# Kernel optimization log

Hardware: AMD Instinct MI355X
Metric: run time of the kernel (lower is better)

## Reference

```python
import jax, jax.numpy as jnp
import numpy as np

NUM_HEADS = 12


def setup_inputs() -> dict:
    key = jax.random.key(0)
    k_x, k_m, k_qkv, k_proj = jax.random.split(key, 4)
    B, N, C = 2, 2048, 768
    x = jax.random.normal(k_x, (B, N, C), dtype=jnp.float32)
    # binary key mask: 1 = attend, 0 = masked out
    mask = jax.random.randint(k_m, (B, N), 0, 2).astype(jnp.int32)
    # torch Linear(dim, dim*3, bias=False): stored here as [in, out]
    w_qkv = jax.random.normal(k_qkv, (C, 3 * C), dtype=jnp.float32) * 0.02
    w_proj = jax.random.normal(k_proj, (C, C), dtype=jnp.float32) * 0.02
    b_proj = jnp.zeros((C,), dtype=jnp.float32)
    return {"x": x, "mask": mask, "w_qkv": w_qkv, "w_proj": w_proj, "b_proj": b_proj}


def reference(x, mask, w_qkv, w_proj, b_proj):
    B, N, C = x.shape
    H = NUM_HEADS
    hd = C // H
    scale = hd ** -0.5
    qkv = (x @ w_qkv).reshape(B, N, 3, H, hd)
    q, k, v = jnp.moveaxis(qkv, 2, 0)            # each [B, N, H, hd]
    attn = jnp.einsum('bnhd,bmhd->bhnm', q, k) * scale  # [B, H, N, N]
    # faithful masked_softmax: unstable exp (no max subtraction), mask keys, renormalize
    m = mask.astype(x.dtype)[:, None, None, :]   # [B, 1, 1, N]
    x_exp = jnp.exp(attn) * m
    attn = x_exp / x_exp.sum(-1, keepdims=True)
    out = jnp.einsum('bhnm,bmhd->bnhd', attn, v).reshape(B, N, C)
    return out @ w_proj + b_proj
```

## Files before the change

kernel.cpp:

```cpp
#include <hip/hip_runtime.h>
#include <cstdint>

#define NB 2
#define NSEQ 2048
#define CDIM 768
#define NH 12
#define HD 64
#define NTOK (NB*NSEQ)
#define QKV_COLS (3*CDIM)
#define NBLK ((NSEQ/64)*NH*NB)

typedef short bf16x8 __attribute__((ext_vector_type(8)));
typedef short bf16x4 __attribute__((ext_vector_type(4)));
typedef float f32x4  __attribute__((ext_vector_type(4)));
typedef short short4v __attribute__((ext_vector_type(4)));
typedef unsigned int uint4v __attribute__((ext_vector_type(4)));

#define MFMA16(a,b,c) __builtin_amdgcn_mfma_f32_16x16x32_bf16(a,b,c,0,0,0)

__device__ __forceinline__ short f2b(float f) {
    uint32_t u = __builtin_bit_cast(uint32_t, f);
    u += 0x7fffu + ((u >> 16) & 1u);
    return (short)(u >> 16);
}
__device__ __forceinline__ unsigned pack2(float a, float b) {
    unsigned ua = __builtin_bit_cast(unsigned, a) + 0x7fffu;
    unsigned ub = __builtin_bit_cast(unsigned, b) + 0x7fffu;
    return __builtin_amdgcn_perm(ub, ua, 0x07060302u);
}
__device__ __forceinline__ void gll16(const short* g, short* l) {
    __builtin_amdgcn_global_load_lds(
        (const __attribute__((address_space(1))) unsigned int*)g,
        (__attribute__((address_space(3))) unsigned int*)l, 16, 0, 0);
}

__global__ __launch_bounds__(256) void prep_kernel(
    const float* __restrict__ x, const float* __restrict__ w_qkv,
    const float* __restrict__ w_proj,
    short* __restrict__ xb, short* __restrict__ wqt, short* __restrict__ wpt)
{
    __shared__ float tile[32][33];
    const int bid = blockIdx.x, t = threadIdx.x;
    if (bid < 3072) {
        int i = bid * 256 + t;
        float4 v = ((const float4*)x)[i];
        short4v o = { f2b(v.x), f2b(v.y), f2b(v.z), f2b(v.w) };
        ((short4v*)xb)[i] = o;
        return;
    }
    const float* w; short* wt; int K, NC, n0, k0;
    if (bid < 3072 + 1728) {
        int r = bid - 3072;
        w = w_qkv; wt = wqt; K = CDIM; NC = QKV_COLS;
        n0 = (r % 72) * 32; k0 = (r / 72) * 32;
    } else {
        int r = bid - 4800;
        w = w_proj; wt = wpt; K = CDIM; NC = CDIM;
        n0 = (r % 24) * 32; k0 = (r / 24) * 32;
    }
    #pragma unroll
    for (int i = 0; i < 4; ++i) {
        int idx = t + i * 256; int r = idx >> 5, c = idx & 31;
        tile[r][c] = w[(size_t)(k0 + r) * NC + n0 + c];
    }
    __syncthreads();
    #pragma unroll
    for (int i = 0; i < 4; ++i) {
        int idx = t + i * 256; int r = idx >> 5, c = idx & 31;
        wt[(size_t)(n0 + r) * K + k0 + c] = f2b(tile[c][r]);
    }
}

__global__ __launch_bounds__(256) void gemm_qkv(
    const short* __restrict__ A ,
    const short* __restrict__ B ,
    short* __restrict__ qb, short* __restrict__ kb, short* __restrict__ vt)
{
    __shared__ short As[128 * 32];
    __shared__ short Bs[128 * 32];
    const int t = threadIdx.x;
    const int lane = t & 63, wid = t >> 6;
    const int quad = lane >> 4, l16 = lane & 15;
    const int wA = wid >> 1, wB = wid & 1;
    const int n0 = blockIdx.x * 128;
    const int m0 = blockIdx.y * 128;

    const int srow = wid * 16 + (lane >> 2), schunk = (lane & 3) * 8;
    const short* ag0 = A + (size_t)(n0 + srow) * CDIM + schunk;
    const short* ag1 = ag0 + (size_t)64 * CDIM;
    const short* bg0 = B + (size_t)(m0 + srow) * CDIM + schunk;
    const short* bg1 = bg0 + (size_t)64 * CDIM;
    short* asl0 = &As[(wid * 16) * 32];
    short* asl1 = &As[(wid * 16 + 64) * 32];
    short* bsl0 = &Bs[(wid * 16) * 32];
    short* bsl1 = &Bs[(wid * 16 + 64) * 32];

    f32x4 acc[4][4] = {};
    for (int k0 = 0; k0 < CDIM; k0 += 32) {
        __syncthreads();
        gll16(ag0 + k0, asl0);
        gll16(ag1 + k0, asl1);
        gll16(bg0 + k0, bsl0);
        gll16(bg1 + k0, bsl1);
        __syncthreads();
        bf16x8 af[4], bf[4];
        #pragma unroll
        for (int i = 0; i < 4; ++i)
            af[i] = *(const bf16x8*)&As[(wA*64 + i*16 + l16) * 32 + quad*8];
        #pragma unroll
        for (int j = 0; j < 4; ++j)
            bf[j] = *(const bf16x8*)&Bs[(wB*64 + j*16 + l16) * 32 + quad*8];
        #pragma unroll
        for (int i = 0; i < 4; ++i)
            #pragma unroll
            for (int j = 0; j < 4; ++j)
                acc[i][j] = MFMA16(af[i], bf[j], acc[i][j]);
    }

    const int colbase = n0 + wA * 64;
    const int s = colbase / CDIM;
    const int h = (colbase - s * CDIM) >> 6;
    const int b = m0 >> 11;
    const size_t bh = (size_t)(b * NH + h);
    const float qsc = (s == 0) ? 0.125f : 1.0f;
    #pragma unroll
    for (int i = 0; i < 4; ++i) {
        const int d0 = i*16 + quad*4;
        #pragma unroll
        for (int j = 0; j < 4; ++j) {
            int tok = (m0 + wB*64 + j*16 + l16) & (NSEQ - 1);
            if (s < 2) {
                short* dst = (s == 0 ? qb : kb) + (bh * NSEQ + tok) * HD + d0;
                short4v o = { f2b(acc[i][j][0] * qsc), f2b(acc[i][j][1] * qsc),
                              f2b(acc[i][j][2] * qsc), f2b(acc[i][j][3] * qsc) };
                *(short4v*)dst = o;
            } else {
                short* dst = vt + (bh * HD + d0) * NSEQ + tok;
                #pragma unroll
                for (int r = 0; r < 4; ++r)
                    dst[(size_t)r * NSEQ] = f2b(acc[i][j][r]);
            }
        }
    }
}

#define STAGE(KT, BUF) do {                                                      \
    short* kb_ = (BUF);                                                          \
    short* vb_ = (BUF) + 8192;                                                   \
    _Pragma("unroll")                                                            \
    for (int j = 0; j < 4; ++j) {                                                \
        gll16(kp + (size_t)((KT) + rK[j]) * HD + cK[j]*8,                        \
              kb_ + wid*2048 + j*512);                                           \
        gll16(vp + (size_t)dV[j] * NSEQ + (KT) + cV[j]*8,                        \
              vb_ + wid*2048 + j*512);                                           \
    }                                                                            \
} while (0)

#define BODY(KT, BUF) do {                                                       \
    const short* KsB_ = (BUF);                                                   \
    const short* VsB_ = (BUF) + 8192;                                            \
    int4 mi0_ = *(const int4*)(mp + (KT) + kbase);                               \
    int4 mi1_ = *(const int4*)(mp + (KT) + 64 + kbase);                          \
    bf16x8 kf00_ = *(const bf16x8*)&KsB_[krow + kc0];                            \
    bf16x8 kf01_ = *(const bf16x8*)&KsB_[krow + kc1];                            \
    bf16x8 kf10_ = *(const bf16x8*)&KsB_[4096 + krow + kc0];                     \
    bf16x8 kf11_ = *(const bf16x8*)&KsB_[4096 + krow + kc1];                     \
    f32x4 s0_[4] = {}, s1_[4] = {};                                              \
    _Pragma("unroll")                                                            \
    for (int jt = 0; jt < 4; ++jt) {                                             \
        s0_[jt] = MFMA16(kf00_, qf[jt][0], s0_[jt]);                             \
        s0_[jt] = MFMA16(kf01_, qf[jt][1], s0_[jt]);                             \
        s1_[jt] = MFMA16(kf10_, qf[jt][0], s1_[jt]);                             \
        s1_[jt] = MFMA16(kf11_, qf[jt][1], s1_[jt]);                             \
    }                                                                            \
    float4 m0_ = {(float)mi0_.x, (float)mi0_.y, (float)mi0_.z, (float)mi0_.w};   \
    float4 m1_ = {(float)mi1_.x, (float)mi1_.y, (float)mi1_.z, (float)mi1_.w};   \
    bf16x8 pb_[4];                                                               \
    _Pragma("unroll")                                                            \
    for (int jt = 0; jt < 4; ++jt) {                                             \
        float e0 = __expf(s0_[jt][0]) * m0_.x;                                   \
        float e1 = __expf(s0_[jt][1]) * m0_.y;                                   \
        float e2 = __expf(s0_[jt][2]) * m0_.z;                                   \
        float e3 = __expf(s0_[jt][3]) * m0_.w;                                   \
        float f0 = __expf(s1_[jt][0]) * m1_.x;                                   \
        float f1 = __expf(s1_[jt][1]) * m1_.y;                                   \
        float f2 = __expf(s1_[jt][2]) * m1_.z;                                   \
        float f3 = __expf(s1_[jt][3]) * m1_.w;                                   \
        l[jt] += ((e0 + e1) + (e2 + e3)) + ((f0 + f1) + (f2 + f3));              \
        uint4v pk_ = { pack2(e0, e1), pack2(e2, e3),                             \
                       pack2(f0, f1), pack2(f2, f3) };                           \
        pb_[jt] = __builtin_bit_cast(bf16x8, pk_);                               \
    }                                                                            \
    _Pragma("unroll")                                                            \
    for (int it = 0; it < 4; ++it) {                                             \
        const int vrow_ = (it*16 + l16) * 128;                                   \
        bf16x4 lo_ = *(const bf16x4*)&VsB_[vrow_ + vposl + vsub];                \
        bf16x4 hi_ = *(const bf16x4*)&VsB_[vrow_ + vposh + vsub];                \
        bf16x8 vf_ = __builtin_shufflevector(lo_, hi_, 0,1,2,3,4,5,6,7);         \
        _Pragma("unroll")                                                        \
        for (int jt = 0; jt < 4; ++jt)                                           \
            o_acc[it][jt] = MFMA16(vf_, pb_[jt], o_acc[it][jt]);                 \
    }                                                                            \
} while (0)

__global__ __launch_bounds__(256, 2) void attn_kernel(
    const short* __restrict__ qb, const short* __restrict__ kb,
    const short* __restrict__ vt, const int* __restrict__ mask,
    short* __restrict__ ao)
{
    __shared__ __align__(16) short KV[2][16384];
    float (*Ob)[68] = (float(*)[68])KV;
    float (*lsum)[64] = (float(*)[64])((char*)KV + 17408);

    const int t = threadIdx.x;
    const int lane = t & 63, wid = t >> 6;
    const int quad = lane >> 4, l16 = lane & 15;
    const int id = blockIdx.x;
    const int idx = id >> 3;
    const int bh = (id & 7) + ((idx % 3) << 3);
    const int q0 = (idx / 3) << 6;
    const int b = bh / NH, h = bh - b * NH;
    const size_t hoff = (size_t)bh * NSEQ * HD;
    const short* qp = qb + hoff;
    const short* kp = kb + hoff;
    const short* vp = vt + hoff;
    const int* mp = mask + b * NSEQ;
    const int kbase = wid * 16 + quad * 4;

    int rK[4], cK[4], dV[4], cV[4];
    #pragma unroll
    for (int j = 0; j < 4; ++j) {
        int o = wid * 4096 + j * 1024 + lane * 16;
        rK[j] = o >> 7;
        cK[j] = ((o >> 4) & 7) ^ (rK[j] & 7);
        dV[j] = o >> 8;
        cV[j] = ((o >> 4) & 15) ^ (dV[j] & 15);
    }
    const int r7 = l16 & 7;
    const int krow = (wid * 16 + l16) * 64;
    const int kc0 = ((quad     ^ r7) << 3);
    const int kc1 = (((quad+4) ^ r7) << 3);
    const int vposl = ((wid*2 + (quad >> 1)) ^ l16) << 3;
    const int vposh = (((8 + wid*2 + (quad >> 1)) ^ l16) << 3);
    const int vsub = (quad & 1) * 4;

    bf16x8 qf[4][2];
    #pragma unroll
    for (int jt = 0; jt < 4; ++jt) {
        const short* qr = qp + (size_t)(q0 + jt*16 + l16) * HD + quad*8;
        qf[jt][0] = *(const bf16x8*)qr;
        qf[jt][1] = *(const bf16x8*)(qr + 32);
    }

    f32x4 o_acc[4][4] = {};
    float l[4] = {0.f, 0.f, 0.f, 0.f};

    STAGE(0, KV[0]);
    __syncthreads();

    for (int kt = 0; kt < NSEQ; kt += 256) {
        STAGE(kt + 128, KV[1]);
        BODY(kt, KV[0]);
        __syncthreads();
        const int nx = (kt + 256) & (NSEQ - 1);
        STAGE(nx, KV[0]);
        BODY(kt + 128, KV[1]);
        __syncthreads();
    }

    #pragma unroll
    for (int jt = 0; jt < 4; ++jt) {
        l[jt] += __shfl_xor(l[jt], 16);
        l[jt] += __shfl_xor(l[jt], 32);
        if (quad == 0) lsum[wid][jt*16 + l16] = l[jt];
    }
    for (int w = 0; w < 4; ++w) {
        __syncthreads();
        if (wid == w) {
            #pragma unroll
            for (int it = 0; it < 4; ++it)
                #pragma unroll
                for (int jt = 0; jt < 4; ++jt)
                    #pragma unroll
                    for (int r = 0; r < 4; ++r) {
                        if (w == 0)
                            Ob[it*16 + quad*4 + r][jt*16 + l16] = o_acc[it][jt][r];
                        else
                            Ob[it*16 + quad*4 + r][jt*16 + l16] += o_acc[it][jt][r];
                    }
        }
    }
    __syncthreads();

    {
        const int ql = t >> 2, dc = (t & 3) * 16;
        float inv = 1.0f / (((lsum[0][ql] + lsum[1][ql]) +
                             (lsum[2][ql] + lsum[3][ql])));
        bf16x8 o8a, o8b;
        #pragma unroll
        for (int d = 0; d < 8; ++d) o8a[d] = f2b(Ob[dc + d][ql] * inv);
        #pragma unroll
        for (int d = 0; d < 8; ++d) o8b[d] = f2b(Ob[dc + 8 + d][ql] * inv);
        int tok = b * NSEQ + q0 + ql;
        short* dst = ao + (size_t)tok * CDIM + h * HD + dc;
        *(bf16x8*)dst = o8a;
        *(bf16x8*)(dst + 8) = o8b;
    }
}

__global__ __launch_bounds__(256) void gemm_proj(
    const short* __restrict__ A ,
    const short* __restrict__ B ,
    const float* __restrict__ bias, float* __restrict__ out)
{
    __shared__ short As[128 * 32];
    __shared__ short Bs[128 * 32];
    const int t = threadIdx.x;
    const int lane = t & 63, wid = t >> 6;
    const int quad = lane >> 4, l16 = lane & 15;
    const int wA = wid >> 1, wB = wid & 1;
    const int n0 = blockIdx.x * 128;
    const int m0 = blockIdx.y * 128;

    const int srow = wid * 16 + (lane >> 2), schunk = (lane & 3) * 8;
    const short* ag0 = A + (size_t)(n0 + srow) * CDIM + schunk;
    const short* ag1 = ag0 + (size_t)64 * CDIM;
    const short* bg0 = B + (size_t)(m0 + srow) * CDIM + schunk;
    const short* bg1 = bg0 + (size_t)64 * CDIM;
    short* asl0 = &As[(wid * 16) * 32];
    short* asl1 = &As[(wid * 16 + 64) * 32];
    short* bsl0 = &Bs[(wid * 16) * 32];
    short* bsl1 = &Bs[(wid * 16 + 64) * 32];

    f32x4 acc[4][4] = {};
    for (int k0 = 0; k0 < CDIM; k0 += 32) {
        __syncthreads();
        gll16(ag0 + k0, asl0);
        gll16(ag1 + k0, asl1);
        gll16(bg0 + k0, bsl0);
        gll16(bg1 + k0, bsl1);
        __syncthreads();
        bf16x8 af[4], bf[4];
        #pragma unroll
        for (int i = 0; i < 4; ++i)
            af[i] = *(const bf16x8*)&As[(wA*64 + i*16 + l16) * 32 + quad*8];
        #pragma unroll
        for (int j = 0; j < 4; ++j)
            bf[j] = *(const bf16x8*)&Bs[(wB*64 + j*16 + l16) * 32 + quad*8];
        #pragma unroll
        for (int i = 0; i < 4; ++i)
            #pragma unroll
            for (int j = 0; j < 4; ++j)
                acc[i][j] = MFMA16(af[i], bf[j], acc[i][j]);
    }

    #pragma unroll
    for (int i = 0; i < 4; ++i) {
        int col0 = n0 + wA*64 + i*16 + quad*4;
        float4 bias4 = *(const float4*)&bias[col0];
        #pragma unroll
        for (int j = 0; j < 4; ++j) {
            int tok = m0 + wB*64 + j*16 + l16;
            float4 o = { acc[i][j][0] + bias4.x, acc[i][j][1] + bias4.y,
                         acc[i][j][2] + bias4.z, acc[i][j][3] + bias4.w };
            *(float4*)(out + (size_t)tok * CDIM + col0) = o;
        }
    }
}

extern "C" void kernel_launch(void* const* d_in, const int* in_sizes, int n_in,
                              void* d_out, int out_size, void* d_ws, size_t ws_size,
                              hipStream_t stream)
{
    const float* x      = (const float*)d_in[0];
    const int*   mask   = (const int*)d_in[1];
    const float* w_qkv  = (const float*)d_in[2];
    const float* w_proj = (const float*)d_in[3];
    const float* b_proj = (const float*)d_in[4];
    float* out = (float*)d_out;

    const size_t SZ = (size_t)NTOK * CDIM;
    short* xb  = (short*)d_ws;
    short* wqt = xb  + SZ;
    short* wpt = wqt + (size_t)QKV_COLS * CDIM;
    short* qb  = wpt + (size_t)CDIM * CDIM;
    short* kb  = qb  + SZ;
    short* vt  = kb  + SZ;
    short* ao  = vt  + SZ;

    dim3 blk(256);
    prep_kernel<<<dim3(5376), blk, 0, stream>>>(x, w_qkv, w_proj, xb, wqt, wpt);
    gemm_qkv<<<dim3(QKV_COLS/128, NTOK/128), blk, 0, stream>>>(wqt, xb, qb, kb, vt);
    attn_kernel<<<dim3(NBLK), blk, 0, stream>>>(qb, kb, vt, mask, ao);
    gemm_proj<<<dim3(CDIM/128, NTOK/128), blk, 0, stream>>>(wpt, ao, b_proj, out);
}
```

Before: 177.1 us.

## Load attention K/V fragments directly from global into registers, drop LDS staging

The attention kernel no longer stages K and V tiles through double-buffered shared memory with async global-to-LDS loads and barriers. Each wave now loads its K fragments straight into registers, double-buffered in software, and reads its V fragments from global memory inside the body. The mask is converted to float once in the prep kernel so the inner loop skips int-to-float conversion. This removes the per-tile __syncthreads and the LDS traffic, at the cost of more global and L2 traffic and higher register pressure, since each wave re-reads K/V that were previously shared across the block.

```diff
diff --git a/kernel.cpp b/kernel.cpp
--- a/kernel.cpp
+++ b/kernel.cpp
@@ -36,8 +36,9 @@
 
 __global__ __launch_bounds__(256) void prep_kernel(
     const float* __restrict__ x, const float* __restrict__ w_qkv,
-    const float* __restrict__ w_proj,
-    short* __restrict__ xb, short* __restrict__ wqt, short* __restrict__ wpt)
+    const float* __restrict__ w_proj, const int* __restrict__ mask,
+    short* __restrict__ xb, short* __restrict__ wqt, short* __restrict__ wpt,
+    float* __restrict__ maskf)
 {
     __shared__ float tile[32][33];
     const int bid = blockIdx.x, t = threadIdx.x;
@@ -46,6 +47,13 @@
         float4 v = ((const float4*)x)[i];
         short4v o = { f2b(v.x), f2b(v.y), f2b(v.z), f2b(v.w) };
         ((short4v*)xb)[i] = o;
+        return;
+    }
+    if (bid >= 5376) {
+        int i = ((bid - 5376) << 10) + (t << 2);
+        int4 mi = *(const int4*)(mask + i);
+        float4 mo = { (float)mi.x, (float)mi.y, (float)mi.z, (float)mi.w };
+        *(float4*)(maskf + i) = mo;
         return;
     }
     const float* w; short* wt; int K, NC, n0, k0;
@@ -144,37 +152,32 @@
     }
 }
 
-#define STAGE(KT, BUF) do {                                                      \
-    short* kb_ = (BUF);                                                          \
-    short* vb_ = (BUF) + 8192;                                                   \
+#define LOADK(KT, KF) do {                                                       \
+    const short* kt_ = kbase + (size_t)(KT) * HD;                                \
+    KF[0] = *(const bf16x8*)(kt_);                                               \
+    KF[1] = *(const bf16x8*)(kt_ + 32);                                          \
+    KF[2] = *(const bf16x8*)(kt_ + 64*HD);                                       \
+    KF[3] = *(const bf16x8*)(kt_ + 64*HD + 32);                                  \
+} while (0)
+
+#define BODY(KT, KF) do {                                                        \
+    bf16x4 vlo_[4], vhi_[4];                                                     \
     _Pragma("unroll")                                                            \
-    for (int j = 0; j < 4; ++j) {                                                \
-        gll16(kp + (size_t)((KT) + rK[j]) * HD + cK[j]*8,                        \
-              kb_ + wid*2048 + j*512);                                           \
-        gll16(vp + (size_t)dV[j] * NSEQ + (KT) + cV[j]*8,                        \
-              vb_ + wid*2048 + j*512);                                           \
+    for (int it = 0; it < 4; ++it) {                                             \
+        const short* vr_ = vbase + (size_t)(it*16) * NSEQ + (KT);                \
+        vlo_[it] = *(const bf16x4*)(vr_);                                        \
+        vhi_[it] = *(const bf16x4*)(vr_ + 64);                                   \
     }                                                                            \
-} while (0)
-
-#define BODY(KT, BUF) do {                                                       \
-    const short* KsB_ = (BUF);                                                   \
-    const short* VsB_ = (BUF) + 8192;                                            \
-    int4 mi0_ = *(const int4*)(mp + (KT) + kbase);                               \
-    int4 mi1_ = *(const int4*)(mp + (KT) + 64 + kbase);                          \
-    bf16x8 kf00_ = *(const bf16x8*)&KsB_[krow + kc0];                            \
-    bf16x8 kf01_ = *(const bf16x8*)&KsB_[krow + kc1];                            \
-    bf16x8 kf10_ = *(const bf16x8*)&KsB_[4096 + krow + kc0];                     \
-    bf16x8 kf11_ = *(const bf16x8*)&KsB_[4096 + krow + kc1];                     \
+    float4 m0_ = *(const float4*)(mp + (KT) + mbase);                            \
+    float4 m1_ = *(const float4*)(mp + (KT) + 64 + mbase);                       \
     f32x4 s0_[4] = {}, s1_[4] = {};                                              \
     _Pragma("unroll")                                                            \
     for (int jt = 0; jt < 4; ++jt) {                                             \
-        s0_[jt] = MFMA16(kf00_, qf[jt][0], s0_[jt]);                             \
-        s0_[jt] = MFMA16(kf01_, qf[jt][1], s0_[jt]);                             \
-        s1_[jt] = MFMA16(kf10_, qf[jt][0], s1_[jt]);                             \
-        s1_[jt] = MFMA16(kf11_, qf[jt][1], s1_[jt]);                             \
+        s0_[jt] = MFMA16(KF[0], qf[jt][0], s0_[jt]);                             \
+        s0_[jt] = MFMA16(KF[1], qf[jt][1], s0_[jt]);                             \
+        s1_[jt] = MFMA16(KF[2], qf[jt][0], s1_[jt]);                             \
+        s1_[jt] = MFMA16(KF[3], qf[jt][1], s1_[jt]);                             \
     }                                                                            \
-    float4 m0_ = {(float)mi0_.x, (float)mi0_.y, (float)mi0_.z, (float)mi0_.w};   \
-    float4 m1_ = {(float)mi1_.x, (float)mi1_.y, (float)mi1_.z, (float)mi1_.w};   \
     bf16x8 pb_[4];                                                               \
     _Pragma("unroll")                                                            \
     for (int jt = 0; jt < 4; ++jt) {                                             \
@@ -193,10 +196,8 @@
     }                                                                            \
     _Pragma("unroll")                                                            \
     for (int it = 0; it < 4; ++it) {                                             \
-        const int vrow_ = (it*16 + l16) * 128;                                   \
-        bf16x4 lo_ = *(const bf16x4*)&VsB_[vrow_ + vposl + vsub];                \
-        bf16x4 hi_ = *(const bf16x4*)&VsB_[vrow_ + vposh + vsub];                \
-        bf16x8 vf_ = __builtin_shufflevector(lo_, hi_, 0,1,2,3,4,5,6,7);         \
+        bf16x8 vf_ = __builtin_shufflevector(vlo_[it], vhi_[it],                 \
+                                             0,1,2,3,4,5,6,7);                   \
         _Pragma("unroll")                                                        \
         for (int jt = 0; jt < 4; ++jt)                                           \
             o_acc[it][jt] = MFMA16(vf_, pb_[jt], o_acc[it][jt]);                 \
@@ -205,12 +206,11 @@
 
 __global__ __launch_bounds__(256, 2) void attn_kernel(
     const short* __restrict__ qb, const short* __restrict__ kb,
-    const short* __restrict__ vt, const int* __restrict__ mask,
+    const short* __restrict__ vt, const float* __restrict__ maskf,
     short* __restrict__ ao)
 {
-    __shared__ __align__(16) short KV[2][16384];
-    float (*Ob)[68] = (float(*)[68])KV;
-    float (*lsum)[64] = (float(*)[64])((char*)KV + 17408);
+    __shared__ __align__(16) float Ob[64][68];
+    __shared__ float lsum[4][64];
 
     const int t = threadIdx.x;
     const int lane = t & 63, wid = t >> 6;
@@ -224,25 +224,11 @@
     const short* qp = qb + hoff;
     const short* kp = kb + hoff;
     const short* vp = vt + hoff;
-    const int* mp = mask + b * NSEQ;
-    const int kbase = wid * 16 + quad * 4;
-
-    int rK[4], cK[4], dV[4], cV[4];
-    #pragma unroll
-    for (int j = 0; j < 4; ++j) {
-        int o = wid * 4096 + j * 1024 + lane * 16;
-        rK[j] = o >> 7;
-        cK[j] = ((o >> 4) & 7) ^ (rK[j] & 7);
-        dV[j] = o >> 8;
-        cV[j] = ((o >> 4) & 15) ^ (dV[j] & 15);
-    }
-    const int r7 = l16 & 7;
-    const int krow = (wid * 16 + l16) * 64;
-    const int kc0 = ((quad     ^ r7) << 3);
-    const int kc1 = (((quad+4) ^ r7) << 3);
-    const int vposl = ((wid*2 + (quad >> 1)) ^ l16) << 3;
-    const int vposh = (((8 + wid*2 + (quad >> 1)) ^ l16) << 3);
-    const int vsub = (quad & 1) * 4;
+    const float* mp = maskf + b * NSEQ;
+    const int mbase = wid * 16 + quad * 4;
+
+    const short* kbase = kp + (size_t)(wid*16 + l16) * HD + quad*8;
+    const short* vbase = vp + (size_t)l16 * NSEQ + wid*16 + quad*4;
 
     bf16x8 qf[4][2];
     #pragma unroll
@@ -255,17 +241,13 @@
     f32x4 o_acc[4][4] = {};
     float l[4] = {0.f, 0.f, 0.f, 0.f};
 
-    STAGE(0, KV[0]);
-    __syncthreads();
-
+    bf16x8 kA[4], kB[4];
+    LOADK(0, kA);
     for (int kt = 0; kt < NSEQ; kt += 256) {
-        STAGE(kt + 128, KV[1]);
-        BODY(kt, KV[0]);
-        __syncthreads();
-        const int nx = (kt + 256) & (NSEQ - 1);
-        STAGE(nx, KV[0]);
-        BODY(kt + 128, KV[1]);
-        __syncthreads();
+        LOADK(kt + 128, kB);
+        BODY(kt, kA);
+        LOADK((kt + 256) & (NSEQ - 1), kA);
+        BODY(kt + 128, kB);
     }
 
     #pragma unroll
@@ -387,10 +369,12 @@
     short* kb  = qb  + SZ;
     short* vt  = kb  + SZ;
     short* ao  = vt  + SZ;
+    float* maskf = (float*)(ao + SZ);
 
     dim3 blk(256);
-    prep_kernel<<<dim3(5376), blk, 0, stream>>>(x, w_qkv, w_proj, xb, wqt, wpt);
+    prep_kernel<<<dim3(5380), blk, 0, stream>>>(x, w_qkv, w_proj, mask,
+                                                xb, wqt, wpt, maskf);
     gemm_qkv<<<dim3(QKV_COLS/128, NTOK/128), blk, 0, stream>>>(wqt, xb, qb, kb, vt);
-    attn_kernel<<<dim3(NBLK), blk, 0, stream>>>(qb, kb, vt, mask, ao);
+    attn_kernel<<<dim3(NBLK), blk, 0, stream>>>(qb, kb, vt, maskf, ao);
     gemm_proj<<<dim3(CDIM/128, NTOK/128), blk, 0, stream>>>(wpt, ao, b_proj, out);
 }
```

Result: slower. 210.0 us (+18.6%).

## Split K/V staging, single-buffer V, cache bf16 mask in LDS for occupancy

Applied to the files above, without the earlier changes.

The attention kernel's shared memory is restructured. K stays double-buffered while V gets a single buffer that is loaded at the start of each tile and consumed after an added barrier. The key mask is converted to bf16 in the prep kernel and staged once per block into LDS, replacing per-tile global int loads. LDS per block drops, so launch bounds rise to 3 blocks per CU for more occupancy. The cost is twice as many barriers per tile and V loads that are now exposed rather than prefetched a tile ahead.

```diff
diff --git a/kernel.cpp b/kernel.cpp
--- a/kernel.cpp
+++ b/kernel.cpp
@@ -23,6 +23,9 @@
     u += 0x7fffu + ((u >> 16) & 1u);
     return (short)(u >> 16);
 }
+__device__ __forceinline__ float b2f(short s) {
+    return __builtin_bit_cast(float, (uint32_t)((uint32_t)(unsigned short)s << 16));
+}
 __device__ __forceinline__ unsigned pack2(float a, float b) {
     unsigned ua = __builtin_bit_cast(unsigned, a) + 0x7fffu;
     unsigned ub = __builtin_bit_cast(unsigned, b) + 0x7fffu;
@@ -36,8 +39,9 @@
 
 __global__ __launch_bounds__(256) void prep_kernel(
     const float* __restrict__ x, const float* __restrict__ w_qkv,
-    const float* __restrict__ w_proj,
-    short* __restrict__ xb, short* __restrict__ wqt, short* __restrict__ wpt)
+    const float* __restrict__ w_proj, const int* __restrict__ mask,
+    short* __restrict__ xb, short* __restrict__ wqt, short* __restrict__ wpt,
+    short* __restrict__ maskb)
 {
     __shared__ float tile[32][33];
     const int bid = blockIdx.x, t = threadIdx.x;
@@ -46,6 +50,18 @@
         float4 v = ((const float4*)x)[i];
         short4v o = { f2b(v.x), f2b(v.y), f2b(v.z), f2b(v.w) };
         ((short4v*)xb)[i] = o;
+        return;
+    }
+    if (bid >= 5376) {
+        int i = ((bid - 5376) << 11) + (t << 3);
+        int4 a = *(const int4*)(mask + i);
+        int4 c = *(const int4*)(mask + i + 4);
+        short4v o0 = { f2b((float)a.x), f2b((float)a.y),
+                       f2b((float)a.z), f2b((float)a.w) };
+        short4v o1 = { f2b((float)c.x), f2b((float)c.y),
+                       f2b((float)c.z), f2b((float)c.w) };
+        *(short4v*)(maskb + i) = o0;
+        *(short4v*)(maskb + i + 4) = o1;
         return;
     }
     const float* w; short* wt; int K, NC, n0, k0;
@@ -144,23 +160,25 @@
     }
 }
 
-#define STAGE(KT, BUF) do {                                                      \
+#define STAGE_K(KT, BUF) do {                                                    \
     short* kb_ = (BUF);                                                          \
-    short* vb_ = (BUF) + 8192;                                                   \
     _Pragma("unroll")                                                            \
-    for (int j = 0; j < 4; ++j) {                                                \
+    for (int j = 0; j < 4; ++j)                                                  \
         gll16(kp + (size_t)((KT) + rK[j]) * HD + cK[j]*8,                        \
               kb_ + wid*2048 + j*512);                                           \
+} while (0)
+
+#define STAGE_V(KT) do {                                                         \
+    _Pragma("unroll")                                                            \
+    for (int j = 0; j < 4; ++j)                                                  \
         gll16(vp + (size_t)dV[j] * NSEQ + (KT) + cV[j]*8,                        \
-              vb_ + wid*2048 + j*512);                                           \
-    }                                                                            \
+              Vb + wid*2048 + j*512);                                            \
 } while (0)
 
-#define BODY(KT, BUF) do {                                                       \
-    const short* KsB_ = (BUF);                                                   \
-    const short* VsB_ = (BUF) + 8192;                                            \
-    int4 mi0_ = *(const int4*)(mp + (KT) + kbase);                               \
-    int4 mi1_ = *(const int4*)(mp + (KT) + 64 + kbase);                          \
+#define QKBODY(KT, KBUF) do {                                                    \
+    const short* KsB_ = (KBUF);                                                  \
+    short4v mi0_ = *(const short4v*)&Msk[(KT) + mbase];                          \
+    short4v mi1_ = *(const short4v*)&Msk[(KT) + 64 + mbase];                     \
     bf16x8 kf00_ = *(const bf16x8*)&KsB_[krow + kc0];                            \
     bf16x8 kf01_ = *(const bf16x8*)&KsB_[krow + kc1];                            \
     bf16x8 kf10_ = *(const bf16x8*)&KsB_[4096 + krow + kc0];                     \
@@ -173,9 +191,8 @@
         s1_[jt] = MFMA16(kf10_, qf[jt][0], s1_[jt]);                             \
         s1_[jt] = MFMA16(kf11_, qf[jt][1], s1_[jt]);                             \
     }                                                                            \
-    float4 m0_ = {(float)mi0_.x, (float)mi0_.y, (float)mi0_.z, (float)mi0_.w};   \
-    float4 m1_ = {(float)mi1_.x, (float)mi1_.y, (float)mi1_.z, (float)mi1_.w};   \
-    bf16x8 pb_[4];                                                               \
+    float4 m0_ = { b2f(mi0_[0]), b2f(mi0_[1]), b2f(mi0_[2]), b2f(mi0_[3]) };     \
+    float4 m1_ = { b2f(mi1_[0]), b2f(mi1_[1]), b2f(mi1_[2]), b2f(mi1_[3]) };     \
     _Pragma("unroll")                                                            \
     for (int jt = 0; jt < 4; ++jt) {                                             \
         float e0 = __expf(s0_[jt][0]) * m0_.x;                                   \
@@ -189,28 +206,33 @@
         l[jt] += ((e0 + e1) + (e2 + e3)) + ((f0 + f1) + (f2 + f3));              \
         uint4v pk_ = { pack2(e0, e1), pack2(e2, e3),                             \
                        pack2(f0, f1), pack2(f2, f3) };                           \
-        pb_[jt] = __builtin_bit_cast(bf16x8, pk_);                               \
+        pb[jt] = __builtin_bit_cast(bf16x8, pk_);                                \
     }                                                                            \
+} while (0)
+
+#define PVBODY() do {                                                            \
     _Pragma("unroll")                                                            \
     for (int it = 0; it < 4; ++it) {                                             \
         const int vrow_ = (it*16 + l16) * 128;                                   \
-        bf16x4 lo_ = *(const bf16x4*)&VsB_[vrow_ + vposl + vsub];                \
-        bf16x4 hi_ = *(const bf16x4*)&VsB_[vrow_ + vposh + vsub];                \
+        bf16x4 lo_ = *(const bf16x4*)&Vb[vrow_ + vposl + vsub];                  \
+        bf16x4 hi_ = *(const bf16x4*)&Vb[vrow_ + vposh + vsub];                  \
         bf16x8 vf_ = __builtin_shufflevector(lo_, hi_, 0,1,2,3,4,5,6,7);         \
         _Pragma("unroll")                                                        \
         for (int jt = 0; jt < 4; ++jt)                                           \
-            o_acc[it][jt] = MFMA16(vf_, pb_[jt], o_acc[it][jt]);                 \
+            o_acc[it][jt] = MFMA16(vf_, pb[jt], o_acc[it][jt]);                  \
     }                                                                            \
 } while (0)
 
-__global__ __launch_bounds__(256, 2) void attn_kernel(
+__global__ __launch_bounds__(256, 3) void attn_kernel(
     const short* __restrict__ qb, const short* __restrict__ kb,
-    const short* __restrict__ vt, const int* __restrict__ mask,
+    const short* __restrict__ vt, const short* __restrict__ maskb,
     short* __restrict__ ao)
 {
-    __shared__ __align__(16) short KV[2][16384];
-    float (*Ob)[68] = (float(*)[68])KV;
-    float (*lsum)[64] = (float(*)[64])((char*)KV + 17408);
+    __shared__ __align__(16) short Kb[2][8192];
+    __shared__ __align__(16) short Vb[8192];
+    __shared__ __align__(16) short Msk[2048];
+    float (*Ob)[68] = (float(*)[68])Kb;
+    float (*lsum)[64] = (float(*)[64])((char*)Kb + 17408);
 
     const int t = threadIdx.x;
     const int lane = t & 63, wid = t >> 6;
@@ -224,8 +246,7 @@
     const short* qp = qb + hoff;
     const short* kp = kb + hoff;
     const short* vp = vt + hoff;
-    const int* mp = mask + b * NSEQ;
-    const int kbase = wid * 16 + quad * 4;
+    const int mbase = wid * 16 + quad * 4;
 
     int rK[4], cK[4], dV[4], cV[4];
     #pragma unroll
@@ -254,17 +275,25 @@
 
     f32x4 o_acc[4][4] = {};
     float l[4] = {0.f, 0.f, 0.f, 0.f};
-
-    STAGE(0, KV[0]);
+    bf16x8 pb[4];
+
+    STAGE_K(0, Kb[0]);
+    gll16(maskb + b * NSEQ + t * 8, Msk + wid * 512);
     __syncthreads();
 
     for (int kt = 0; kt < NSEQ; kt += 256) {
-        STAGE(kt + 128, KV[1]);
-        BODY(kt, KV[0]);
-        __syncthreads();
-        const int nx = (kt + 256) & (NSEQ - 1);
-        STAGE(nx, KV[0]);
-        BODY(kt + 128, KV[1]);
+        STAGE_V(kt);
+        STAGE_K(kt + 128, Kb[1]);
+        QKBODY(kt, Kb[0]);
+        __syncthreads();
+        PVBODY();
+        __syncthreads();
+
+        STAGE_V(kt + 128);
+        STAGE_K((kt + 256) & (NSEQ - 1), Kb[0]);
+        QKBODY(kt + 128, Kb[1]);
+        __syncthreads();
+        PVBODY();
         __syncthreads();
     }
 
@@ -387,10 +416,12 @@
     short* kb  = qb  + SZ;
     short* vt  = kb  + SZ;
     short* ao  = vt  + SZ;
+    short* maskb = ao + SZ;
 
     dim3 blk(256);
-    prep_kernel<<<dim3(5376), blk, 0, stream>>>(x, w_qkv, w_proj, xb, wqt, wpt);
+    prep_kernel<<<dim3(5378), blk, 0, stream>>>(x, w_qkv, w_proj, mask,
+                                                xb, wqt, wpt, maskb);
     gemm_qkv<<<dim3(QKV_COLS/128, NTOK/128), blk, 0, stream>>>(wqt, xb, qb, kb, vt);
-    attn_kernel<<<dim3(NBLK), blk, 0, stream>>>(qb, kb, vt, mask, ao);
+    attn_kernel<<<dim3(NBLK), blk, 0, stream>>>(qb, kb, vt, maskb, ao);
     gemm_proj<<<dim3(CDIM/128, NTOK/128), blk, 0, stream>>>(wpt, ao, b_proj, out);
 }
```

Measured after the change: 273.9 us. 54.7% more time.
